# Kernel optimization log

Measured on AMD Instinct MI355X. Metric: run time of the kernel, lower is better.

The kernel has to match this reference:

```python
import jax, jax.numpy as jnp
import numpy as np

B, D, E, K = 16384, 1024, 8, 2  # tokens, embed_size, experts, top-k
W_IMPORTANCE = 0.01


def setup_inputs() -> dict:
    key = jax.random.key(0)
    ks = jax.random.split(key, 8)
    s = 1.0 / np.sqrt(D)
    return {
        "x": jax.random.normal(ks[0], (B, D), dtype=jnp.float32),   # fused vision features
        "q": jax.random.normal(ks[1], (B, D), dtype=jnp.float32),   # text features
        # cross-attention (seq_len=1) collapses to V then output projection
        "Wv": jax.random.normal(ks[2], (D, D), dtype=jnp.float32) * s,
        "bv": jnp.zeros((D,), dtype=jnp.float32),
        "Wo": jax.random.normal(ks[3], (D, D), dtype=jnp.float32) * s,
        "bo": jnp.zeros((D,), dtype=jnp.float32),
        # gate linear
        "Wg": jax.random.normal(ks[4], (D, E), dtype=jnp.float32) * s,
        "bg": jnp.zeros((E,), dtype=jnp.float32),
        # experts: Linear -> SiLU -> Linear
        "W1": jax.random.normal(ks[5], (E, D, D), dtype=jnp.float32) * s,
        "b1": jnp.zeros((E, D), dtype=jnp.float32),
        "W2": jax.random.normal(ks[6], (E, D, D), dtype=jnp.float32) * s,
        "b2": jnp.zeros((E, D), dtype=jnp.float32),
    }


def reference(x, q, Wv, bv, Wo, bo, Wg, bg, W1, b1, W2, b2):
    # CrossAttention with q_len = kv_len = 1: softmax over a single key is 1,
    # so attention output = out_proj(V(q)).
    att = (q @ Wv + bv) @ Wo + bo                      # (B, D)
    gate_logits = att @ Wg + bg                        # (B, E)
    gate_prob = jax.nn.softmax(gate_logits, axis=-1)   # eval mode: no noise
    top_w, top_i = jax.lax.top_k(gate_prob, K)         # (B, K)
    top_w = jax.nn.softmax(top_w, axis=-1)             # renormalize over top-k

    y = jnp.zeros_like(x)
    for e in range(E):  # small fixed expert count
        w_e = jnp.sum(jnp.where(top_i == e, top_w, 0.0), axis=-1)  # (B,)
        h = jax.nn.silu(x @ W1[e] + b1[e]) @ W2[e] + b2[e]         # (B, D)
        y = y + w_e[:, None] * h

    importance = gate_prob.sum(axis=0)  # (E,)
    importance_loss = W_IMPORTANCE * (jnp.std(importance, ddof=1) / jnp.mean(importance)) ** 2
    return y, gate_prob, importance_loss
```

## Files before the change

### kernel.cpp

```cpp
#include <hip/hip_runtime.h>
#include <hip/hip_bf16.h>

#define Btok 16384
#define Ddim 1024
#define Eexp 8

typedef __attribute__((ext_vector_type(8))) short short8;
typedef __attribute__((ext_vector_type(4))) float f32x4;

__device__ inline unsigned short f2bf(float f) {
    unsigned int u = __float_as_uint(f);
    unsigned int r = (u + 0x7fffu + ((u >> 16) & 1u)) >> 16;
    return (unsigned short)r;
}

__device__ inline void gload16(const void* g, void* l) {
    __builtin_amdgcn_global_load_lds(
        (const __attribute__((address_space(1))) void*)g,
        (__attribute__((address_space(3))) void*)l, 16, 0, 0);
}

__global__ __launch_bounds__(256) void k_tmp(const float* __restrict__ Wo,
                                             const float* __restrict__ Wg,
                                             float* __restrict__ tmp) {
    int id = blockIdx.x * 256 + threadIdx.x;
    int d = id >> 3, e = id & 7;
    double s = 0.0;
    for (int k = 0; k < Ddim; ++k)
        s += (double)Wo[(long)d * Ddim + k] * (double)Wg[k * Eexp + e];
    tmp[id] = (float)s;
}

__global__ __launch_bounds__(256) void k_wc(const float* __restrict__ Wv,
                                            const float* __restrict__ tmp,
                                            float* __restrict__ WcT) {
    int id = blockIdx.x * 256 + threadIdx.x;
    int d = id >> 3, e = id & 7;
    double s = 0.0;
    for (int k = 0; k < Ddim; ++k)
        s += (double)Wv[(long)d * Ddim + k] * (double)tmp[k * Eexp + e];
    WcT[e * Ddim + d] = (float)s;
}

__global__ __launch_bounds__(512) void k_bc(const float* __restrict__ bv,
                                            const float* __restrict__ bo,
                                            const float* __restrict__ bg,
                                            const float* __restrict__ Wg,
                                            const float* __restrict__ tmp,
                                            float* __restrict__ bcomb) {
    int w = threadIdx.x >> 6, l = threadIdx.x & 63;
    double s = 0.0;
    for (int k = l; k < Ddim; k += 64)
        s += (double)bv[k] * (double)tmp[k * Eexp + w] +
             (double)bo[k] * (double)Wg[k * Eexp + w];
    #pragma unroll
    for (int off = 32; off; off >>= 1) s += __shfl_xor(s, off);
    if (l == 0) bcomb[w] = (float)s + bg[w];
}

__global__ __launch_bounds__(256) void k_convx(const float4* __restrict__ x,
                                               ushort4* __restrict__ xb) {
    int i = blockIdx.x * 256 + threadIdx.x;
    float4 v = x[i];
    ushort4 o;
    o.x = f2bf(v.x); o.y = f2bf(v.y); o.z = f2bf(v.z); o.w = f2bf(v.w);
    xb[i] = o;
}

__global__ __launch_bounds__(256) void k_convw(const float* __restrict__ W1,
                                               const float* __restrict__ W2,
                                               unsigned short* __restrict__ w1bT,
                                               unsigned short* __restrict__ w2bT) {
    __shared__ float tile[32][33];
    int bid = blockIdx.x;
    int arr = bid >> 13;
    int e = (bid >> 10) & 7, bi = (bid >> 5) & 31, bj = bid & 31;
    const float* src = (arr ? W2 : W1) + (long)e * Ddim * Ddim;
    unsigned short* dst = (arr ? w2bT : w1bT) + (long)e * Ddim * Ddim;
    int tr = threadIdx.x >> 5, tc = threadIdx.x & 31;
    #pragma unroll
    for (int i = 0; i < 4; ++i) {
        int dl = tr + i * 8;
        tile[dl][tc] = src[(long)(bi * 32 + dl) * Ddim + bj * 32 + tc];
    }
    __syncthreads();
    #pragma unroll
    for (int i = 0; i < 4; ++i) {
        int nl = tr + i * 8;
        dst[(long)(bj * 32 + nl) * Ddim + bi * 32 + tc] = f2bf(tile[tc][nl]);
    }
}

__global__ __launch_bounds__(256) void k_gate(const float* __restrict__ q,
                                              const float* __restrict__ WcT,
                                              const float* __restrict__ bcomb,
                                              float* __restrict__ gate_prob,
                                              int* __restrict__ choice,
                                              float2* __restrict__ w12,
                                              float* __restrict__ impP) {
    __shared__ float impL[4][8];
    int w = threadIdx.x >> 6, l = threadIdx.x & 63;
    int t = blockIdx.x * 4 + w;
    const float* qr = q + (long)t * Ddim;
    float acc[8] = {0, 0, 0, 0, 0, 0, 0, 0};
    #pragma unroll
    for (int i = 0; i < 4; ++i) {
        float4 qv = *(const float4*)(qr + (i * 64 + l) * 4);
        #pragma unroll
        for (int e = 0; e < 8; ++e) {
            float4 wv = *(const float4*)(WcT + e * Ddim + (i * 64 + l) * 4);
            acc[e] += qv.x * wv.x + qv.y * wv.y + qv.z * wv.z + qv.w * wv.w;
        }
    }
    #pragma unroll
    for (int off = 32; off; off >>= 1)
        #pragma unroll
        for (int e = 0; e < 8; ++e) acc[e] += __shfl_xor(acc[e], off);
    float lg[8], p[8];
    float m = -1e30f;
    #pragma unroll
    for (int e = 0; e < 8; ++e) { lg[e] = acc[e] + bcomb[e]; m = fmaxf(m, lg[e]); }
    float s = 0.f;
    #pragma unroll
    for (int e = 0; e < 8; ++e) { p[e] = expf(lg[e] - m); s += p[e]; }
    float inv = 1.f / s;
    #pragma unroll
    for (int e = 0; e < 8; ++e) p[e] *= inv;
    float p1 = -1.f, p2 = -1.f; int i1 = 0, i2 = 0;
    #pragma unroll
    for (int e = 0; e < 8; ++e) {
        float pe = p[e];
        if (pe > p1) { p2 = p1; i2 = i1; p1 = pe; i1 = e; }
        else if (pe > p2) { p2 = pe; i2 = e; }
    }
    float ee = expf(p2 - p1);
    float wa = 1.f / (1.f + ee);
    float wb = ee / (1.f + ee);
    if (l == 0) {
        #pragma unroll
        for (int e = 0; e < 8; ++e) gate_prob[(long)t * 8 + e] = p[e];
        #pragma unroll
        for (int e = 0; e < 8; ++e) impL[w][e] = p[e];
        choice[t] = i1 | (i2 << 8);
        w12[t] = make_float2(wa, wb);
    }
    __syncthreads();
    if (threadIdx.x < 8)
        impP[blockIdx.x * 8 + threadIdx.x] =
            impL[0][threadIdx.x] + impL[1][threadIdx.x] +
            impL[2][threadIdx.x] + impL[3][threadIdx.x];
}

__global__ __launch_bounds__(256) void k_route(const int* __restrict__ choice,
                                               const float2* __restrict__ w12,
                                               int* __restrict__ counts,
                                               int* __restrict__ tok,
                                               float* __restrict__ wgt) {
    __shared__ int cnt[8];
    __shared__ int base[8];
    if (threadIdx.x < 8) cnt[threadIdx.x] = 0;
    __syncthreads();
    int t = blockIdx.x * 256 + threadIdx.x;
    int ch = choice[t];
    int i1 = ch & 255, i2 = ch >> 8;
    float2 ww = w12[t];
    int lp1 = atomicAdd(&cnt[i1], 1);
    int lp2 = atomicAdd(&cnt[i2], 1);
    __syncthreads();
    if (threadIdx.x < 8)
        base[threadIdx.x] = atomicAdd(&counts[threadIdx.x], cnt[threadIdx.x]);
    __syncthreads();
    int p1 = base[i1] + lp1;
    tok[i1 * Btok + p1] = t; wgt[i1 * Btok + p1] = ww.x;
    int p2 = base[i2] + lp2;
    tok[i2 * Btok + p2] = t; wgt[i2 * Btok + p2] = ww.y;
}

template <int MODE>
__global__ __launch_bounds__(256, 4) void k_gemm(const unsigned short* __restrict__ Abase,
                                                 const unsigned short* __restrict__ WT,
                                                 const float* __restrict__ bias,
                                                 const int* __restrict__ counts,
                                                 const int* __restrict__ tok,
                                                 const float* __restrict__ wgt,
                                                 unsigned short* __restrict__ Hout,
                                                 float* __restrict__ y) {
    __shared__ __align__(16) char lds[32768];
    char* ldsp = (char*)lds;

    int bid = blockIdx.x;
    int e = bid & 7;
    int k = bid >> 3;
    int rt = k >> 3, ct = k & 7;

    int n_e = counts[e];
    int r0 = rt * 128;
    if (r0 >= n_e) return;
    int off_e = 0;
    #pragma unroll
    for (int j = 0; j < 8; ++j) off_e += (j < e) ? counts[j] : 0;
    int n0 = ct * 128;

    int t = threadIdx.x;
    int w = t >> 6, l = t & 63;
    int wm = w >> 1, wn = w & 1;

    int tr = t >> 3;
    int sc = (t & 7) ^ (tr & 7);
    const char* srcA[4]; const char* srcB[4];
    #pragma unroll
    for (int ri = 0; ri < 4; ++ri) {
        int idx = r0 + ri * 32 + tr; if (idx > n_e - 1) idx = n_e - 1;
        long g = (MODE == 0) ? (long)tok[e * Btok + idx] : (long)(off_e + idx);
        srcA[ri] = (const char*)Abase + g * 2048 + sc * 16;
        srcB[ri] = (const char*)WT + ((long)e << 21) + (long)(n0 + ri * 32 + tr) * 2048 + sc * 16;
    }
    int dstoff = tr * 128 + (t & 7) * 16;

    int rA = (wm * 64 + (l & 15)) * 128;
    int rB = (wn * 64 + (l & 15)) * 128;
    int x0 = ((l >> 4) ^ (l & 7)) << 4;
    int x1 = (((l >> 4) + 4) ^ (l & 7)) << 4;

    f32x4 acc[4][4];
    #pragma unroll
    for (int mi = 0; mi < 4; ++mi)
        #pragma unroll
        for (int ni = 0; ni < 4; ++ni) acc[mi][ni] = {0.f, 0.f, 0.f, 0.f};

    const int NT = Ddim / 64;
    for (int kk = 0; kk < NT; ++kk) {
        #pragma unroll
        for (int ri = 0; ri < 4; ++ri) {
            gload16(srcA[ri], ldsp + ri * 4096 + dstoff);
            gload16(srcB[ri], ldsp + 16384 + ri * 4096 + dstoff);
            srcA[ri] += 128; srcB[ri] += 128;
        }
        __syncthreads();
        #pragma unroll
        for (int ks = 0; ks < 2; ++ks) {
            int xo = ks ? x1 : x0;
            short8 av[4], bv[4];
            #pragma unroll
            for (int mi = 0; mi < 4; ++mi)
                av[mi] = *(const short8*)(ldsp + rA + mi * 2048 + xo);
            #pragma unroll
            for (int ni = 0; ni < 4; ++ni)
                bv[ni] = *(const short8*)(ldsp + 16384 + rB + ni * 2048 + xo);
            #pragma unroll
            for (int mi = 0; mi < 4; ++mi)
                #pragma unroll
                for (int ni = 0; ni < 4; ++ni)
                    acc[mi][ni] = __builtin_amdgcn_mfma_f32_16x16x32_bf16(av[mi], bv[ni], acc[mi][ni], 0, 0, 0);
        }
        __syncthreads();
    }

    float bias4[4];
    #pragma unroll
    for (int ni = 0; ni < 4; ++ni)
        bias4[ni] = bias[e * Ddim + n0 + wn * 64 + ni * 16 + (l & 15)];

    #pragma unroll
    for (int mi = 0; mi < 4; ++mi) {
        #pragma unroll
        for (int j = 0; j < 4; ++j) {
            int rl = wm * 64 + mi * 16 + (l >> 4) * 4 + j;
            int r = r0 + rl;
            bool ok = r < n_e;
            int trow = 0; float wr = 0.f;
            if (MODE == 1) {
                int ri = ok ? r : 0;
                trow = tok[e * Btok + ri];
                wr = wgt[e * Btok + ri];
            }
            #pragma unroll
            for (int ni = 0; ni < 4; ++ni) {
                int col = n0 + wn * 64 + ni * 16 + (l & 15);
                float v = acc[mi][ni][j] + bias4[ni];
                if (MODE == 0) {
                    v = v / (1.f + __expf(-v));
                    if (ok) Hout[(long)(off_e + r) * Ddim + col] = f2bf(v);
                } else {
                    if (ok) atomicAdd(&y[(long)trow * Ddim + col], wr * v);
                }
            }
        }
    }
}

__global__ __launch_bounds__(256) void k_loss(const float* __restrict__ impP,
                                              float* __restrict__ out) {
    __shared__ float red[256];
    __shared__ float impF[8];
    for (int e = 0; e < 8; ++e) {
        float s = 0.f;
        for (int i = threadIdx.x; i < 4096; i += 256) s += impP[i * 8 + e];
        red[threadIdx.x] = s;
        __syncthreads();
        for (int st = 128; st > 0; st >>= 1) {
            if ((int)threadIdx.x < st) red[threadIdx.x] += red[threadIdx.x + st];
            __syncthreads();
        }
        if (threadIdx.x == 0) impF[e] = red[0];
        __syncthreads();
    }
    if (threadIdx.x == 0) {
        double mean = 0.0;
        for (int e = 0; e < 8; ++e) mean += (double)impF[e];
        mean /= 8.0;
        double var = 0.0;
        for (int e = 0; e < 8; ++e) {
            double d = (double)impF[e] - mean;
            var += d * d;
        }
        var /= 7.0;
        out[0] = (float)(0.01 * var / (mean * mean));
    }
}

extern "C" void kernel_launch(void* const* d_in, const int* in_sizes, int n_in,
                              void* d_out, int out_size, void* d_ws, size_t ws_size,
                              hipStream_t stream) {
    const float* x  = (const float*)d_in[0];
    const float* q  = (const float*)d_in[1];
    const float* Wv = (const float*)d_in[2];
    const float* bv = (const float*)d_in[3];
    const float* Wo = (const float*)d_in[4];
    const float* bo = (const float*)d_in[5];
    const float* Wg = (const float*)d_in[6];
    const float* bg = (const float*)d_in[7];
    const float* W1 = (const float*)d_in[8];
    const float* b1 = (const float*)d_in[9];
    const float* W2 = (const float*)d_in[10];
    const float* b2 = (const float*)d_in[11];

    float* y = (float*)d_out;
    float* gate_prob = y + (long)Btok * Ddim;
    float* loss = gate_prob + (long)Btok * Eexp;

    char* ws = (char*)d_ws;
    int*   counts = (int*)(ws + 0);
    float* bcomb  = (float*)(ws + 256);
    float* tmp    = (float*)(ws + 512);
    float* WcT    = (float*)(ws + 33280);
    float* impP   = (float*)(ws + 66048);
    int*   choice = (int*)(ws + 197120);
    float2* w12   = (float2*)(ws + 262656);
    int*   tok    = (int*)(ws + 393728);
    float* wgt    = (float*)(ws + 918016);
    unsigned short* xb   = (unsigned short*)(ws + 1442304);
    unsigned short* w1bT = (unsigned short*)(ws + 34996736);
    unsigned short* w2bT = (unsigned short*)(ws + 51773952);
    unsigned short* H    = (unsigned short*)(ws + 68551168);

    hipMemsetAsync(counts, 0, 32, stream);
    hipMemsetAsync(y, 0, (size_t)Btok * Ddim * sizeof(float), stream);

    k_tmp<<<32, 256, 0, stream>>>(Wo, Wg, tmp);
    k_wc <<<32, 256, 0, stream>>>(Wv, tmp, WcT);
    k_bc <<<1, 512, 0, stream>>>(bv, bo, bg, Wg, tmp, bcomb);
    k_convx<<<16384, 256, 0, stream>>>((const float4*)x, (ushort4*)xb);
    k_convw<<<16384, 256, 0, stream>>>(W1, W2, w1bT, w2bT);
    k_gate<<<4096, 256, 0, stream>>>(q, WcT, bcomb, gate_prob, choice, w12, impP);
    k_route<<<64, 256, 0, stream>>>(choice, w12, counts, tok, wgt);
    k_gemm<0><<<4096, 256, 0, stream>>>(xb, w1bT, b1, counts, tok, wgt, H, nullptr);
    k_gemm<1><<<4096, 256, 0, stream>>>(H, w2bT, b2, counts, tok, wgt, nullptr, y);
    k_loss<<<1, 256, 0, stream>>>(impP, loss);
}
```

Measured before the change: 454.4 us.

## Make expert routing deterministic and order-preserving, and swizzle GEMM tile order

Replaces the single atomic-based routing kernel with a histogram, a prefix scan and a ballot-based scatter, so each expert's token list stays in ascending token order rather than atomic arrival order. This should make the gathered rows in each GEMM tile more contiguous and gives a deterministic layout. The GEMM block-to-tile mapping is also regrouped so concurrently running blocks share row and column tiles, improving L2 reuse. The cost is two extra small kernel launches and a loop of eight block-wide barriers in the scatter.

```diff
diff --git a/kernel.cpp b/kernel.cpp
--- a/kernel.cpp
+++ b/kernel.cpp
@@ -151,29 +151,61 @@
             impL[2][threadIdx.x] + impL[3][threadIdx.x];
 }
 
-__global__ __launch_bounds__(256) void k_route(const int* __restrict__ choice,
-                                               const float2* __restrict__ w12,
-                                               int* __restrict__ counts,
-                                               int* __restrict__ tok,
-                                               float* __restrict__ wgt) {
+__global__ __launch_bounds__(256) void k_hist(const int* __restrict__ choice,
+                                              int* __restrict__ bcnt) {
     __shared__ int cnt[8];
-    __shared__ int base[8];
     if (threadIdx.x < 8) cnt[threadIdx.x] = 0;
     __syncthreads();
+    int ch = choice[blockIdx.x * 256 + threadIdx.x];
+    atomicAdd(&cnt[ch & 255], 1);
+    atomicAdd(&cnt[(ch >> 8) & 255], 1);
+    __syncthreads();
+    if (threadIdx.x < 8) bcnt[blockIdx.x * 8 + threadIdx.x] = cnt[threadIdx.x];
+}
+
+__global__ __launch_bounds__(512) void k_scan(const int* __restrict__ bcnt,
+                                              int* __restrict__ bbase,
+                                              int* __restrict__ counts) {
+    int w = threadIdx.x >> 6, l = threadIdx.x & 63;
+    int v = bcnt[l * 8 + w];
+    int s = v;
+    #pragma unroll
+    for (int off = 1; off < 64; off <<= 1) {
+        int o = __shfl_up(s, off);
+        if (l >= off) s += o;
+    }
+    bbase[l * 8 + w] = s - v;
+    if (l == 63) counts[w] = s;
+}
+
+__global__ __launch_bounds__(256) void k_scatter(const int* __restrict__ choice,
+                                                 const float2* __restrict__ w12,
+                                                 const int* __restrict__ bbase,
+                                                 int* __restrict__ tok,
+                                                 float* __restrict__ wgt) {
+    __shared__ int wsum[4];
+    int w = threadIdx.x >> 6, l = threadIdx.x & 63;
     int t = blockIdx.x * 256 + threadIdx.x;
     int ch = choice[t];
-    int i1 = ch & 255, i2 = ch >> 8;
+    int i1 = ch & 255, i2 = (ch >> 8) & 255;
     float2 ww = w12[t];
-    int lp1 = atomicAdd(&cnt[i1], 1);
-    int lp2 = atomicAdd(&cnt[i2], 1);
-    __syncthreads();
-    if (threadIdx.x < 8)
-        base[threadIdx.x] = atomicAdd(&counts[threadIdx.x], cnt[threadIdx.x]);
-    __syncthreads();
-    int p1 = base[i1] + lp1;
-    tok[i1 * Btok + p1] = t; wgt[i1 * Btok + p1] = ww.x;
-    int p2 = base[i2] + lp2;
-    tok[i2 * Btok + p2] = t; wgt[i2 * Btok + p2] = ww.y;
+    for (int e = 0; e < 8; ++e) {
+        bool f1 = (i1 == e), f2 = (i2 == e);
+        bool f = f1 || f2;
+        unsigned long long m = __ballot(f);
+        int wl = __popcll(m & ((1ull << l) - 1ull));
+        if (l == 0) wsum[w] = (int)__popcll(m);
+        __syncthreads();
+        int before = 0;
+        #pragma unroll
+        for (int j = 0; j < 4; ++j) before += (j < w) ? wsum[j] : 0;
+        if (f) {
+            int p = bbase[blockIdx.x * 8 + e] + before + wl;
+            tok[e * Btok + p] = t;
+            wgt[e * Btok + p] = f1 ? ww.x : ww.y;
+        }
+        __syncthreads();
+    }
 }
 
 template <int MODE>
@@ -191,7 +223,10 @@
     int bid = blockIdx.x;
     int e = bid & 7;
     int k = bid >> 3;
-    int rt = k >> 3, ct = k & 7;
+    int group = k >> 5;
+    int inner = k & 31;
+    int rt = (group >> 1) * 8 + (inner & 7);
+    int ct = (group & 1) * 4 + (inner >> 3);
 
     int n_e = counts[e];
     int r0 = rt * 128;
@@ -349,12 +384,13 @@
     float2* w12   = (float2*)(ws + 262656);
     int*   tok    = (int*)(ws + 393728);
     float* wgt    = (float*)(ws + 918016);
-    unsigned short* xb   = (unsigned short*)(ws + 1442304);
-    unsigned short* w1bT = (unsigned short*)(ws + 34996736);
-    unsigned short* w2bT = (unsigned short*)(ws + 51773952);
-    unsigned short* H    = (unsigned short*)(ws + 68551168);
-
-    hipMemsetAsync(counts, 0, 32, stream);
+    int*   bcnt   = (int*)(ws + 1442304);
+    int*   bbase  = (int*)(ws + 1444352);
+    unsigned short* xb   = (unsigned short*)(ws + 1446912);
+    unsigned short* w1bT = (unsigned short*)(ws + 35001344);
+    unsigned short* w2bT = (unsigned short*)(ws + 51778560);
+    unsigned short* H    = (unsigned short*)(ws + 68555776);
+
     hipMemsetAsync(y, 0, (size_t)Btok * Ddim * sizeof(float), stream);
 
     k_tmp<<<32, 256, 0, stream>>>(Wo, Wg, tmp);
@@ -363,7 +399,9 @@
     k_convx<<<16384, 256, 0, stream>>>((const float4*)x, (ushort4*)xb);
     k_convw<<<16384, 256, 0, stream>>>(W1, W2, w1bT, w2bT);
     k_gate<<<4096, 256, 0, stream>>>(q, WcT, bcomb, gate_prob, choice, w12, impP);
-    k_route<<<64, 256, 0, stream>>>(choice, w12, counts, tok, wgt);
+    k_hist<<<64, 256, 0, stream>>>(choice, bcnt);
+    k_scan<<<1, 512, 0, stream>>>(bcnt, bbase, counts);
+    k_scatter<<<64, 256, 0, stream>>>(choice, w12, bbase, tok, wgt);
     k_gemm<0><<<4096, 256, 0, stream>>>(xb, w1bT, b1, counts, tok, wgt, H, nullptr);
     k_gemm<1><<<4096, 256, 0, stream>>>(H, w2bT, b2, counts, tok, wgt, nullptr, y);
     k_loss<<<1, 256, 0, stream>>>(impP, loss);
```

New measurement: 456.2 us. No clear change (+0.4%).
